# Performance work log

Hardware: AMD Instinct MI355X
Metric: run time of the kernel (lower is better)

## Reference

```python
import jax, jax.numpy as jnp
import numpy as np

D_MODEL = 1024
D_FF = 8192
N_ELEM = 64            # d2 (elements per block)
D1 = D_FF // N_ELEM    # 128 block rows
BATCH = 2048


def setup_inputs() -> dict:
    key = jax.random.key(0)
    k1, k2, k3, k4, k5 = jax.random.split(key, 5)
    # xavier-uniform-like init for w1 (d_model, d_ff) -> view (d_model, d1, d2)
    bound1 = float(np.sqrt(6.0 / (D_MODEL + D_FF)))
    w1 = jax.random.uniform(k1, (D_MODEL, D1, N_ELEM), jnp.float32, -bound1, bound1)
    # w2 (d_ff, d_model) -> view (d2, d1, d_model); kernel_scaling=True multiplies by sqrt(d2)
    w2 = jax.random.uniform(k2, (N_ELEM, D1, D_MODEL), jnp.float32, -bound1, bound1)
    w2 = w2 * (N_ELEM ** 0.5)
    b2 = jax.random.normal(k3, (D_MODEL,), jnp.float32)
    x = jax.random.normal(k4, (BATCH, D_MODEL), jnp.float32)
    quant_mask = jax.random.randint(k5, (BATCH, D1), 0, N_ELEM, jnp.int32)
    return {"quant_mask": quant_mask, "x": x, "w1": w1, "w2": w2, "b2": b2}


def reference(quant_mask, x, w1, w2, b2):
    # predict-mode path of SparseFFMain (multiply_by_controller_output=False)
    d1 = w1.shape[1]
    w1p = jnp.transpose(w1, (1, 2, 0))   # (d1, d2, d_model)
    w2p = jnp.transpose(w2, (1, 0, 2))   # (d1, d2, d_model)
    rows = jnp.arange(d1)[None, :]        # (1, d1) broadcasts over batch
    # per-sample gathered expert sub-blocks: (B, d1, d_model)
    w = w1p[rows, quant_mask]
    v = w2p[rows, quant_mask]
    mid = jnp.einsum('bd,bjd->bj', x, w)   # (B, d1)
    relu = jax.nn.relu(mid)
    res = jnp.einsum('bj,bjd->bd', relu, v) + b2  # (B, d_model)
    return (quant_mask, res)
```

## Files before the change

### kernel.cpp

```cpp
#include <hip/hip_runtime.h>

#define D_MODEL 1024
#define D_FF    8192
#define N_ELEM  64
#define D1      128
#define BATCH   2048
#define B_T     8
#define NJT     8
#define JT      16

typedef unsigned short u16;
typedef unsigned int   u32;
typedef _Float16 h2    __attribute__((ext_vector_type(2)));
typedef float    f32x4 __attribute__((ext_vector_type(4)));
typedef u32      u32x2 __attribute__((ext_vector_type(2)));

__device__ __forceinline__ h2 as_h2(u32 u) { union { u32 i; h2 h; } c; c.i = u; return c.h; }
__device__ __forceinline__ u32 pkh(float a, float b) {
    union { h2 h; u32 u; } c; c.h.x = (_Float16)a; c.h.y = (_Float16)b; return c.u;
}
__device__ __forceinline__ u16 f2h(float f) {
    union { _Float16 h; u16 u; } c; c.h = (_Float16)f; return c.u;
}
__device__ __forceinline__ f32x4 ntload4(const float* p) {
    return __builtin_nontemporal_load((const f32x4*)p);
}

__global__ __launch_bounds__(256) void transpose_cast_w1(const float* __restrict__ w1,
                                                         u16* __restrict__ w1h) {
    __shared__ float tile[64][65];
    const int c0 = blockIdx.x * 64;
    const int d0 = blockIdx.y * 64;
    const int tx = threadIdx.x & 15;
    const int ty = threadIdx.x >> 4;
#pragma unroll
    for (int r = 0; r < 4; ++r) {
        const int row = ty * 4 + r;
        const float4 v = *(const float4*)(w1 + (size_t)(d0 + row) * D_FF + c0 + tx * 4);
        tile[row][tx * 4 + 0] = v.x;
        tile[row][tx * 4 + 1] = v.y;
        tile[row][tx * 4 + 2] = v.z;
        tile[row][tx * 4 + 3] = v.w;
    }
    __syncthreads();
#pragma unroll
    for (int r = 0; r < 4; ++r) {
        const int c = ty * 4 + r;
        ushort4 o;
        o.x = f2h(tile[tx * 4 + 0][c]);
        o.y = f2h(tile[tx * 4 + 1][c]);
        o.z = f2h(tile[tx * 4 + 2][c]);
        o.w = f2h(tile[tx * 4 + 3][c]);
        *(ushort4*)(w1h + (size_t)(c0 + c) * D_MODEL + d0 + tx * 4) = o;
    }
}

__global__ __launch_bounds__(256) void cast_w2(const float* __restrict__ w2,
                                               u16* __restrict__ w2h) {
    const size_t i = ((size_t)blockIdx.x * 256 + threadIdx.x) * 8;
    const float4 a = *(const float4*)(w2 + i);
    const float4 b = *(const float4*)(w2 + i + 4);
    ushort4 oa, ob;
    oa.x = f2h(a.x); oa.y = f2h(a.y); oa.z = f2h(a.z); oa.w = f2h(a.w);
    ob.x = f2h(b.x); ob.y = f2h(b.y); ob.z = f2h(b.z); ob.w = f2h(b.w);
    *(ushort4*)(w2h + i)     = oa;
    *(ushort4*)(w2h + i + 4) = ob;
}

__global__ __launch_bounds__(256) void sparse_ff_jt(const int* __restrict__ mask,
                                                    const float* __restrict__ x,
                                                    const u16* __restrict__ w1h_,
                                                    const u16* __restrict__ w2h_,
                                                    u16* __restrict__ part) {
    const _Float16* w1h = (const _Float16*)w1h_;
    const _Float16* w2h = (const _Float16*)w2h_;
    __shared__ float r_lds[B_T][JT];
    __shared__ int   m_lds[B_T][JT];

    const int jt = blockIdx.x & (NJT - 1);
    const int b0 = (blockIdx.x >> 3) * B_T;
    const int t = threadIdx.x;
    const int wave = t >> 6;
    const int lane = t & 63;

    if (t < B_T * JT) {
        m_lds[t >> 4][t & 15] = mask[(b0 + (t >> 4)) * D1 + jt * JT + (t & 15)];
    }
    __syncthreads();

#pragma unroll
    for (int rep = 0; rep < 2; ++rep) {
        const int bi = wave * 2 + rep;
        const float* xrow = x + (size_t)(b0 + bi) * D_MODEL;
        const f32x4 xa0 = ntload4(xrow + lane * 8);
        const f32x4 xa1 = ntload4(xrow + lane * 8 + 4);
        const f32x4 xb0 = ntload4(xrow + 512 + lane * 8);
        const f32x4 xb1 = ntload4(xrow + 512 + lane * 8 + 4);
        float xr[16];
        *(f32x4*)&xr[0]  = xa0; *(f32x4*)&xr[4]  = xa1;
        *(f32x4*)&xr[8]  = xb0; *(f32x4*)&xr[12] = xb1;

        for (int jj = 0; jj < JT; jj += 4) {
            const int j0 = jt * JT + jj;
            uint4 wa[4], wb[4];
#pragma unroll
            for (int q = 0; q < 4; ++q) {
                const _Float16* col = w1h
                    + (size_t)(((j0 + q) << 6) + m_lds[bi][jj + q]) * D_MODEL;
                wa[q] = *(const uint4*)(col + lane * 8);
                wb[q] = *(const uint4*)(col + 512 + lane * 8);
            }
            float s[4];
#pragma unroll
            for (int q = 0; q < 4; ++q) {
                const u32 w[8] = {wa[q].x, wa[q].y, wa[q].z, wa[q].w,
                                  wb[q].x, wb[q].y, wb[q].z, wb[q].w};
                float a = 0.f;
#pragma unroll
                for (int k = 0; k < 8; ++k) {
                    const h2 p = as_h2(w[k]);
                    a = fmaf((float)p.x, xr[2 * k], a);
                    a = fmaf((float)p.y, xr[2 * k + 1], a);
                }
                s[q] = a;
            }
#pragma unroll
            for (int off = 32; off; off >>= 1) {
                s[0] += __shfl_down(s[0], off);
                s[1] += __shfl_down(s[1], off);
                s[2] += __shfl_down(s[2], off);
                s[3] += __shfl_down(s[3], off);
            }
            if (lane == 0) {
                r_lds[bi][jj]     = fmaxf(s[0], 0.f);
                r_lds[bi][jj + 1] = fmaxf(s[1], 0.f);
                r_lds[bi][jj + 2] = fmaxf(s[2], 0.f);
                r_lds[bi][jj + 3] = fmaxf(s[3], 0.f);
            }
        }
    }
    __syncthreads();

    const int d0q = t * 4;
    for (int bi = 0; bi < B_T; ++bi) {
        float a0 = 0.f, a1 = 0.f, a2 = 0.f, a3 = 0.f;
        for (int jj = 0; jj < JT; ++jj) {
            const float r = r_lds[bi][jj];
            if (r > 0.f) {
                const _Float16* row = w2h
                    + (size_t)(m_lds[bi][jj] * D1 + jt * JT + jj) * D_MODEL + d0q;
                const uint2 v = *(const uint2*)row;
                const h2 p0 = as_h2(v.x), p1 = as_h2(v.y);
                a0 = fmaf(r, (float)p0.x, a0); a1 = fmaf(r, (float)p0.y, a1);
                a2 = fmaf(r, (float)p1.x, a2); a3 = fmaf(r, (float)p1.y, a3);
            }
        }
        u32x2 o;
        o.x = pkh(a0, a1);
        o.y = pkh(a2, a3);
        u16* pp = part + ((size_t)jt * BATCH + (b0 + bi)) * D_MODEL + d0q;
        __builtin_nontemporal_store(o, (u32x2*)pp);
    }
}

__global__ __launch_bounds__(256) void reduce_partials(const int* __restrict__ mask,
                                                       const float* __restrict__ b2,
                                                       const u16* __restrict__ part,
                                                       float* __restrict__ out) {
    const int b = blockIdx.x;
    const int t = threadIdx.x;
    if (t < D1) out[(size_t)b * D1 + t] = (float)mask[b * D1 + t];

    const int d0 = t * 4;
    const float4 bv = *(const float4*)(b2 + d0);
    float a0 = bv.x, a1 = bv.y, a2 = bv.z, a3 = bv.w;
#pragma unroll
    for (int jt = 0; jt < NJT; ++jt) {
        const uint2 v = *(const uint2*)(part + ((size_t)jt * BATCH + b) * D_MODEL + d0);
        const h2 p0 = as_h2(v.x), p1 = as_h2(v.y);
        a0 += (float)p0.x; a1 += (float)p0.y;
        a2 += (float)p1.x; a3 += (float)p1.y;
    }
    *(float4*)(out + (size_t)BATCH * D1 + (size_t)b * D_MODEL + d0) =
        make_float4(a0, a1, a2, a3);
}

__global__ __launch_bounds__(256) void sparse_ff_f32_raw(const int* __restrict__ mask,
                                                         const float* __restrict__ x,
                                                         const float* __restrict__ w1,
                                                         const float* __restrict__ w2,
                                                         const float* __restrict__ b2,
                                                         float* __restrict__ out) {
    __shared__ float x_lds[D_MODEL];
    __shared__ float relu_lds[D1];
    __shared__ int   m_lds[D1];
    const int b = blockIdx.x, t = threadIdx.x;
    const int wave = t >> 6, lane = t & 63;
    *(float4*)&x_lds[t * 4] = *(const float4*)(x + (size_t)b * D_MODEL + t * 4);
    if (t < D1) {
        const int mv = mask[b * D1 + t];
        m_lds[t] = mv;
        out[(size_t)b * D1 + t] = (float)mv;
    }
    __syncthreads();
    for (int jj = 0; jj < 32; ++jj) {
        const int j = wave * 32 + jj;
        const int m = m_lds[j];
        float acc = 0.f;
#pragma unroll
        for (int c = 0; c < 16; ++c) {
            const int d = c * 64 + lane;
            acc = fmaf(w1[(size_t)d * D_FF + j * N_ELEM + m], x_lds[d], acc);
        }
#pragma unroll
        for (int off = 32; off; off >>= 1) acc += __shfl_down(acc, off);
        if (lane == 0) relu_lds[j] = fmaxf(acc, 0.f);
    }
    __syncthreads();
    const int dm0 = t * 4;
    const float4 bv = *(const float4*)(b2 + dm0);
    float a0 = bv.x, a1 = bv.y, a2 = bv.z, a3 = bv.w;
    for (int j = 0; j < D1; ++j) {
        const float r = relu_lds[j];
        if (r > 0.f) {
            const float4 wv = *(const float4*)(w2 + (size_t)(m_lds[j] * D1 + j) * D_MODEL + dm0);
            a0 = fmaf(r, wv.x, a0); a1 = fmaf(r, wv.y, a1);
            a2 = fmaf(r, wv.z, a2); a3 = fmaf(r, wv.w, a3);
        }
    }
    *(float4*)(out + (size_t)BATCH * D1 + (size_t)b * D_MODEL + dm0) =
        make_float4(a0, a1, a2, a3);
}

extern "C" void kernel_launch(void* const* d_in, const int* in_sizes, int n_in,
                              void* d_out, int out_size, void* d_ws, size_t ws_size,
                              hipStream_t stream) {
    const int*   mask = (const int*)d_in[0];
    const float* x    = (const float*)d_in[1];
    const float* w1   = (const float*)d_in[2];
    const float* w2   = (const float*)d_in[3];
    const float* b2   = (const float*)d_in[4];
    float* out = (float*)d_out;

    const size_t w1h_bytes  = (size_t)D_FF * D_MODEL * sizeof(u16);
    const size_t w2h_bytes  = (size_t)D_FF * D_MODEL * sizeof(u16);
    const size_t part_bytes = (size_t)NJT * BATCH * D_MODEL * sizeof(u16);

    if (ws_size >= w1h_bytes + w2h_bytes + part_bytes) {
        u16* w1h  = (u16*)d_ws;
        u16* w2h  = (u16*)((char*)d_ws + w1h_bytes);
        u16* part = (u16*)((char*)d_ws + w1h_bytes + w2h_bytes);
        transpose_cast_w1<<<dim3(D_FF / 64, D_MODEL / 64), 256, 0, stream>>>(w1, w1h);
        cast_w2<<<(D_FF * D_MODEL / 8) / 256, 256, 0, stream>>>(w2, w2h);
        sparse_ff_jt<<<(BATCH / B_T) * NJT, 256, 0, stream>>>(mask, x, w1h, w2h, part);
        reduce_partials<<<BATCH, 256, 0, stream>>>(mask, b2, part, out);
    } else {
        sparse_ff_f32_raw<<<BATCH, 256, 0, stream>>>(mask, x, w1, w2, b2, out);
    }
}
```

Before: 208.5 us.

## Batch wave reductions through padded LDS transpose and unroll second-stage loop

Instead of a 6-step shuffle reduction per group of four columns, each wave accumulates all 16 column partials in registers, writes them to a padded LDS buffer, and reduces them with a transposed 16-element sum plus two xor shuffles. The second stage preloads relu values and mask indices into registers with vector LDS reads and fully unrolls the column loop so loads can issue earlier. Launch bounds now request 4 blocks per CU, and the new 16.6KB LDS buffer and extra registers may limit occupancy or cause spills.

```diff
diff --git a/kernel.cpp b/kernel.cpp
--- a/kernel.cpp
+++ b/kernel.cpp
@@ -8,6 +8,7 @@
 #define B_T     8
 #define NJT     8
 #define JT      16
+#define RSTRIDE 65
 
 typedef unsigned short u16;
 typedef unsigned int   u32;
@@ -67,13 +68,14 @@
     *(ushort4*)(w2h + i + 4) = ob;
 }
 
-__global__ __launch_bounds__(256) void sparse_ff_jt(const int* __restrict__ mask,
-                                                    const float* __restrict__ x,
-                                                    const u16* __restrict__ w1h_,
-                                                    const u16* __restrict__ w2h_,
-                                                    u16* __restrict__ part) {
+__global__ __launch_bounds__(256, 4) void sparse_ff_jt(const int* __restrict__ mask,
+                                                       const float* __restrict__ x,
+                                                       const u16* __restrict__ w1h_,
+                                                       const u16* __restrict__ w2h_,
+                                                       u16* __restrict__ part) {
     const _Float16* w1h = (const _Float16*)w1h_;
     const _Float16* w2h = (const _Float16*)w2h_;
+    __shared__ float red[4][JT * RSTRIDE];
     __shared__ float r_lds[B_T][JT];
     __shared__ int   m_lds[B_T][JT];
 
@@ -100,55 +102,68 @@
         *(f32x4*)&xr[0]  = xa0; *(f32x4*)&xr[4]  = xa1;
         *(f32x4*)&xr[8]  = xb0; *(f32x4*)&xr[12] = xb1;
 
+        float s[16];
+#pragma unroll
+        for (int i = 0; i < 16; ++i) s[i] = 0.f;
+
+#pragma unroll
         for (int jj = 0; jj < JT; jj += 4) {
-            const int j0 = jt * JT + jj;
             uint4 wa[4], wb[4];
 #pragma unroll
             for (int q = 0; q < 4; ++q) {
                 const _Float16* col = w1h
-                    + (size_t)(((j0 + q) << 6) + m_lds[bi][jj + q]) * D_MODEL;
+                    + (size_t)(((jt * JT + jj + q) << 6) + m_lds[bi][jj + q]) * D_MODEL;
                 wa[q] = *(const uint4*)(col + lane * 8);
                 wb[q] = *(const uint4*)(col + 512 + lane * 8);
             }
-            float s[4];
 #pragma unroll
             for (int q = 0; q < 4; ++q) {
                 const u32 w[8] = {wa[q].x, wa[q].y, wa[q].z, wa[q].w,
                                   wb[q].x, wb[q].y, wb[q].z, wb[q].w};
-                float a = 0.f;
+                float a = s[jj + q];
 #pragma unroll
                 for (int k = 0; k < 8; ++k) {
                     const h2 p = as_h2(w[k]);
                     a = fmaf((float)p.x, xr[2 * k], a);
                     a = fmaf((float)p.y, xr[2 * k + 1], a);
                 }
-                s[q] = a;
+                s[jj + q] = a;
             }
-#pragma unroll
-            for (int off = 32; off; off >>= 1) {
-                s[0] += __shfl_down(s[0], off);
-                s[1] += __shfl_down(s[1], off);
-                s[2] += __shfl_down(s[2], off);
-                s[3] += __shfl_down(s[3], off);
-            }
-            if (lane == 0) {
-                r_lds[bi][jj]     = fmaxf(s[0], 0.f);
-                r_lds[bi][jj + 1] = fmaxf(s[1], 0.f);
-                r_lds[bi][jj + 2] = fmaxf(s[2], 0.f);
-                r_lds[bi][jj + 3] = fmaxf(s[3], 0.f);
-            }
-        }
+        }
+
+#pragma unroll
+        for (int j = 0; j < 16; ++j) red[wave][j * RSTRIDE + lane] = s[j];
+        const int q = lane >> 4, jr = lane & 15;
+        const float* rb = &red[wave][jr * RSTRIDE + q * 16];
+        float v = 0.f;
+#pragma unroll
+        for (int i = 0; i < 16; ++i) v += rb[i];
+        v += __shfl_xor(v, 16, 64);
+        v += __shfl_xor(v, 32, 64);
+        if (lane < 16) r_lds[bi][lane] = fmaxf(v, 0.f);
     }
     __syncthreads();
 
     const int d0q = t * 4;
     for (int bi = 0; bi < B_T; ++bi) {
+        float rr[16];
+        *(f32x4*)&rr[0]  = *(const f32x4*)&r_lds[bi][0];
+        *(f32x4*)&rr[4]  = *(const f32x4*)&r_lds[bi][4];
+        *(f32x4*)&rr[8]  = *(const f32x4*)&r_lds[bi][8];
+        *(f32x4*)&rr[12] = *(const f32x4*)&r_lds[bi][12];
+        int mr[16];
+#pragma unroll
+        for (int i = 0; i < 16; i += 4) {
+            const int4 mv = *(const int4*)&m_lds[bi][i];
+            mr[i] = mv.x; mr[i + 1] = mv.y; mr[i + 2] = mv.z; mr[i + 3] = mv.w;
+        }
         float a0 = 0.f, a1 = 0.f, a2 = 0.f, a3 = 0.f;
-        for (int jj = 0; jj < JT; ++jj) {
-            const float r = r_lds[bi][jj];
+#pragma unroll
+        for (int jj = 0; jj < 16; ++jj) {
+            const float r = rr[jj];
             if (r > 0.f) {
                 const _Float16* row = w2h
-                    + (size_t)(m_lds[bi][jj] * D1 + jt * JT + jj) * D_MODEL + d0q;
+                    + (size_t)(mr[jj] * D1 + jt * JT + jj) * D_MODEL + d0q;
                 const uint2 v = *(const uint2*)row;
                 const h2 p0 = as_h2(v.x), p1 = as_h2(v.y);
                 a0 = fmaf(r, (float)p0.x, a0); a1 = fmaf(r, (float)p0.y, a1);
```

Result: faster. 199.6 us (-4.3%).
